# Performance work log

Measured on AMD Instinct MI355X. Metric: run time of the kernel, lower is better.

## Reference

```python
import math
import jax, jax.numpy as jnp
import numpy as np

HIDDEN = 256
FREQ = 256          # frequency_embedding_size
MASK_RATIO = 0.75
B, L, PD = 16, 4096, 512  # batch, num_patches, patch_dim = 2*16*16


def setup_inputs() -> dict:
    key = jax.random.key(0)
    ks = jax.random.split(key, 12)
    patches = jax.random.normal(ks[0], (B, L, PD), jnp.float32)
    # sorted segment ids -> contiguous segments per row (bincount/cumsum structure)
    sample_ids = jnp.sort(jax.random.randint(ks[1], (B, L), 0, 8), axis=1).astype(jnp.int32)
    effective_lens = (jax.random.randint(ks[2], (B,), 0, 2048) + L // 2).astype(jnp.int32)
    noise = jax.random.uniform(ks[3], (B, L), dtype=jnp.float32)
    fs = jax.random.uniform(ks[4], (B,), dtype=jnp.float32) * 1000.0
    W = jax.random.normal(ks[5], (HIDDEN, PD), jnp.float32) * 0.02   # projection.weight
    b = jnp.zeros((HIDDEN,), jnp.float32)                            # projection.bias
    pos = jax.random.normal(ks[6], (L, HIDDEN), jnp.float32) * 0.02  # position_embeddings
    w1 = jax.random.normal(ks[7], (HIDDEN, FREQ), jnp.float32) * 0.02
    b1 = jnp.zeros((HIDDEN,), jnp.float32)
    w2 = jax.random.normal(ks[8], (HIDDEN, HIDDEN), jnp.float32) * 0.02
    b2 = jnp.zeros((HIDDEN,), jnp.float32)
    return {"patches": patches, "sample_ids": sample_ids,
            "effective_lens": effective_lens, "noise": noise, "fs": fs,
            "W": W, "b": b, "pos": pos, "w1": w1, "b1": b1, "w2": w2, "b2": b2}


def timestep_embedding(t, dim=FREQ, max_period=10000.0):
    half = dim // 2
    freqs = jnp.exp(-math.log(max_period) * jnp.arange(half, dtype=jnp.float32) / half)
    args = t[:, None] * freqs[None, :]
    return jnp.concatenate([jnp.cos(args), jnp.sin(args)], axis=-1)  # [B, FREQ]


def reference(patches, sample_ids, effective_lens, noise, fs,
              W, b, pos, w1, b1, w2, b2):
    Bb, Ll, _ = patches.shape
    # patch projection + position embeddings
    emb = jnp.einsum('blp,hp->blh', patches, W) + b + pos[None]  # [B, L, H]
    # timestep (fs) embedding: Linear -> SiLU -> Linear
    t_freq = timestep_embedding(fs)
    fs_emb = jax.nn.silu(t_freq @ w1.T + b1) @ w2.T + b2  # [B, H]

    j = jnp.arange(Ll)[None, :]
    valid = j < effective_lens[:, None]                       # key-pad mask
    prev = jnp.concatenate([jnp.full((Bb, 1), -1, sample_ids.dtype),
                            sample_ids[:, :-1]], axis=1)
    seg_start = valid & (sample_ids != prev)                  # cls-token slots
    fs_tok = valid & jnp.concatenate([jnp.zeros((Bb, 1), bool),
                                      seg_start[:, :-1]], axis=1)  # fs-token slots
    # prefix (cls+fs) tokens get noise 0 -> always kept; padding -> inf
    nz = jnp.where(seg_start | fs_tok, 0.0, noise)
    nz = jnp.where(valid, nz, jnp.inf)

    num_samples = seg_start.sum(axis=1).astype(jnp.int32)
    keep_f = (effective_lens - 2 * num_samples).astype(jnp.float32) * (1.0 - MASK_RATIO)
    len_keep = 2 * num_samples + jnp.trunc(keep_f).astype(jnp.int32)

    ids_shuffle = jnp.argsort(nz, axis=1)                     # [B, L]
    keep = j < len_keep[:, None]
    # partial re-sort: sort first len_keep kept indices per row
    prefix_sorted = jnp.sort(jnp.where(keep, ids_shuffle, Ll), axis=1)
    ids_shuffle = jnp.where(keep, prefix_sorted, ids_shuffle)
    ids_restore = jnp.argsort(ids_shuffle, axis=1)

    gathered = jnp.take_along_axis(emb, ids_shuffle[..., None], axis=1)
    # fs conditioning added to kept tokens; padded (to L, masked) beyond len_keep
    seq_unmasked = jnp.where(keep[..., None], gathered + fs_emb[:, None, :], 0.0)

    mae_base = ((j >= len_keep[:, None]) & valid).astype(jnp.float32)
    mae_mask = jnp.take_along_axis(mae_base, ids_restore, axis=1)
    # fa2 path: no dense attn mask, just segment ids of kept tokens
    unmask_ids = jnp.where(keep,
                           jnp.take_along_axis(sample_ids, ids_shuffle, axis=1), -1)
    return seq_unmasked, mae_mask, ids_restore, unmask_ids
```

## Files before the change

### kernel.cpp

```cpp
#include <hip/hip_runtime.h>
#include <hip/hip_bf16.h>

#define BB 16
#define LL 4096
#define PDIM 512
#define HH 256
#define HALFD 128
#define MT 32

typedef short bf16x8 __attribute__((ext_vector_type(8)));
typedef float f32x4 __attribute__((ext_vector_type(4)));

__device__ __forceinline__ unsigned short f2bf(float f) {
  unsigned x = __float_as_uint(f);
  unsigned r = (x + 0x7FFFu + ((x >> 16) & 1u)) >> 16;
  return (unsigned short)r;
}

__device__ __forceinline__ unsigned long long make_key(
    const int* __restrict__ sid, const float* __restrict__ nrow, int eff, int j) {
  int s = sid[j];
  int sp = (j >= 1) ? sid[j - 1] : -1;
  int spp = (j >= 2) ? sid[j - 2] : -1;
  bool valid = j < eff;
  bool segs = valid && (s != sp);
  bool fst = valid && (j > 0) && (sp != spp);
  unsigned vb;
  if (!valid) vb = 0x7F800000u;
  else if (segs || fst) vb = 0u;
  else vb = __float_as_uint(nrow[j]);
  return (((unsigned long long)vb) << 32) | (unsigned)j;
}

__global__ __launch_bounds__(256) void prep_kernel(
    const float* __restrict__ W, unsigned short* __restrict__ Wbf,
    const float* __restrict__ fs, const float* __restrict__ w1,
    const float* __restrict__ b1, const float* __restrict__ w2,
    const float* __restrict__ b2, float* __restrict__ fs_emb) {
  __shared__ float tf[HH];
  __shared__ float hid[HH];
  if (blockIdx.x < 512) {
    int idx = blockIdx.x * 256 + threadIdx.x;
    Wbf[idx] = f2bf(W[idx]);
    return;
  }
  const int b = blockIdx.x - 512, h = threadIdx.x;
  float fv = fs[b];
  int i = h & (HALFD - 1);
  float freq = expf(-9.210340371976184f * (float)i / 128.0f);
  float arg = fv * freq;
  tf[h] = (h < HALFD) ? cosf(arg) : sinf(arg);
  __syncthreads();
  float acc = b1[h];
  const float* wr = w1 + (size_t)h * HH;
  for (int k = 0; k < HH; k += 4) {
    float4 w4 = *reinterpret_cast<const float4*>(&wr[k]);
    acc += tf[k] * w4.x + tf[k + 1] * w4.y + tf[k + 2] * w4.z + tf[k + 3] * w4.w;
  }
  hid[h] = acc / (1.0f + expf(-acc));
  __syncthreads();
  float acc2 = b2[h];
  const float* wr2 = w2 + (size_t)h * HH;
  for (int k = 0; k < HH; k += 4) {
    float4 w4 = *reinterpret_cast<const float4*>(&wr2[k]);
    acc2 += hid[k] * w4.x + hid[k + 1] * w4.y + hid[k + 2] * w4.z + hid[k + 3] * w4.w;
  }
  fs_emb[b * HH + h] = acc2;
}

__global__ __launch_bounds__(512) void rank_kernel(
    const int* __restrict__ sample_ids, const int* __restrict__ eff_lens,
    const float* __restrict__ noise, int* __restrict__ rank_part) {
  const int oq = blockIdx.x, os = blockIdx.y, b = blockIdx.z, tid = threadIdx.x;
  __shared__ __align__(16) unsigned long long sk[1024];
  const int eff = eff_lens[b];
  const int* sid = sample_ids + (size_t)b * LL;
  const float* nrow = noise + (size_t)b * LL;

  sk[tid] = make_key(sid, nrow, eff, os * 1024 + tid);
  sk[tid + 512] = make_key(sid, nrow, eff, os * 1024 + tid + 512);
  const int e0 = oq * 1024 + tid * 2;
  const unsigned long long k0 = make_key(sid, nrow, eff, e0);
  const unsigned long long k1 = make_key(sid, nrow, eff, e0 + 1);
  __syncthreads();

  int c0 = 0, c1 = 0;
#pragma unroll 8
  for (int k = 0; k < 1024; k += 2) {
    ulonglong2 kk = *reinterpret_cast<const ulonglong2*>(&sk[k]);
    c0 += (kk.x < k0) ? 1 : 0;
    c0 += (kk.y < k0) ? 1 : 0;
    c1 += (kk.x < k1) ? 1 : 0;
    c1 += (kk.y < k1) ? 1 : 0;
  }
  int2 res = make_int2(c0, c1);
  *reinterpret_cast<int2*>(&rank_part[((size_t)os * BB + b) * LL + e0]) = res;
}

__global__ __launch_bounds__(1024) void finalize_kernel(
    const int* __restrict__ sample_ids, const int* __restrict__ eff_lens,
    const int* __restrict__ rank_part, float* __restrict__ out_mae,
    float* __restrict__ out_restore, float* __restrict__ out_unmask,
    int* __restrict__ keep_idx, int* __restrict__ lk_arr) {
  const int b = blockIdx.x, tid = threadIdx.x;
  const int wid = tid >> 6, lane = tid & 63;
  __shared__ int wsum[16];
  __shared__ int lksh;
  const int eff = eff_lens[b];
  const int* sid = sample_ids + (size_t)b * LL;

  int local_ns = 0;
  for (int j = tid; j < LL; j += 1024) {
    int s = sid[j];
    int sp = (j >= 1) ? sid[j - 1] : -1;
    if (j < eff && s != sp) local_ns++;
  }
#pragma unroll
  for (int off = 32; off > 0; off >>= 1) local_ns += __shfl_down(local_ns, off);
  if (lane == 0) wsum[wid] = local_ns;
  __syncthreads();
  if (wid == 0) {
    int v = (lane < 16) ? wsum[lane] : 0;
#pragma unroll
    for (int off = 32; off > 0; off >>= 1) v += __shfl_down(v, off);
    if (lane == 0) {
      int ns = v;
      lksh = 2 * ns + ((eff - 2 * ns) >> 2);
    }
  }
  __syncthreads();
  const int lk = lksh;

  const int base = tid * 4;
  int4 p0 = *reinterpret_cast<const int4*>(&rank_part[((size_t)0 * BB + b) * LL + base]);
  int4 p1 = *reinterpret_cast<const int4*>(&rank_part[((size_t)1 * BB + b) * LL + base]);
  int4 p2 = *reinterpret_cast<const int4*>(&rank_part[((size_t)2 * BB + b) * LL + base]);
  int4 p3 = *reinterpret_cast<const int4*>(&rank_part[((size_t)3 * BB + b) * LL + base]);
  int r4[4] = {p0.x + p1.x + p2.x + p3.x, p0.y + p1.y + p2.y + p3.y,
               p0.z + p1.z + p2.z + p3.z, p0.w + p1.w + p2.w + p3.w};
  int c4[4], cnt = 0;
#pragma unroll
  for (int q = 0; q < 4; ++q) { c4[q] = (r4[q] < lk) ? 1 : 0; cnt += c4[q]; }

  int incl = cnt;
#pragma unroll
  for (int off = 1; off < 64; off <<= 1) {
    int v = __shfl_up(incl, off);
    if (lane >= off) incl += v;
  }
  if (lane == 63) wsum[wid] = incl;
  __syncthreads();
  if (wid == 0) {
    int s = (lane < 16) ? wsum[lane] : 0;
#pragma unroll
    for (int off = 1; off < 16; off <<= 1) {
      int v = __shfl_up(s, off);
      if (lane >= off) s += v;
    }
    if (lane < 16) wsum[lane] = s;
  }
  __syncthreads();
  int run = ((wid > 0) ? wsum[wid - 1] : 0) + incl - cnt;

  float4 rst, mmk;
  float* rp = &rst.x; float* mp = &mmk.x;
#pragma unroll
  for (int q = 0; q < 4; ++q) {
    int j = base + q;
    int r;
    if (c4[q]) {
      r = run;
      keep_idx[b * LL + run] = j;
      out_unmask[(size_t)b * LL + run] = (float)sid[j];
      run++;
    } else {
      r = r4[q];
    }
    rp[q] = (float)r;
    mp[q] = (r >= lk && r < eff) ? 1.0f : 0.0f;
  }
  *reinterpret_cast<float4*>(out_restore + (size_t)b * LL + base) = rst;
  *reinterpret_cast<float4*>(out_mae + (size_t)b * LL + base) = mmk;

  for (int p = tid; p < LL; p += 1024)
    if (p >= lk) out_unmask[(size_t)b * LL + p] = -1.0f;
  if (tid == 0) lk_arr[b] = lk;
}

__global__ __launch_bounds__(256) void proj_kernel(
    const float* __restrict__ patches, const unsigned short* __restrict__ Wbf,
    const float* __restrict__ bias, const float* __restrict__ pos,
    const float* __restrict__ fs_emb, const int* __restrict__ keep_idx,
    const int* __restrict__ lk_arr, float* __restrict__ out0) {
  const int tile = blockIdx.x, b = blockIdx.y, tid = threadIdx.x;
  const int p0 = tile * MT;
  int lk = lk_arr[b];
  lk = lk < 0 ? 0 : (lk > LL ? LL : lk);
  float* outB = out0 + ((size_t)b * LL + p0) * HH;
  int nt = lk - p0;
  nt = nt > MT ? MT : nt;

  if (nt <= 0) {
    float4 z = make_float4(0.f, 0.f, 0.f, 0.f);
    float4* o4 = reinterpret_cast<float4*>(outB);
#pragma unroll
    for (int i = 0; i < MT * HH / 4 / 256; ++i)
      o4[i * 256 + tid] = z;
    return;
  }

  __shared__ __align__(16) unsigned short pA[MT * 520];
  __shared__ int idxs[MT];
  if (tid < MT) idxs[tid] = (tid < nt) ? (keep_idx[b * LL + p0 + tid] & (LL - 1)) : 0;
  __syncthreads();

  {
    const int r = tid >> 3, kc = (tid & 7) * 64;
    const float* prow = patches + ((size_t)b * LL + (size_t)idxs[r]) * PDIM + kc;
#pragma unroll
    for (int i = 0; i < 16; ++i) {
      float4 v = reinterpret_cast<const float4*>(prow)[i];
      ushort4 u = make_ushort4(f2bf(v.x), f2bf(v.y), f2bf(v.z), f2bf(v.w));
      *reinterpret_cast<ushort4*>(&pA[r * 520 + kc + i * 4]) = u;
    }
  }
  __syncthreads();

  const int lane = tid & 63, w = tid >> 6;
  const int li = lane & 15, q = lane >> 4;
  f32x4 zero4 = {0.f, 0.f, 0.f, 0.f};
  f32x4 acc[2][4];
#pragma unroll
  for (int m = 0; m < 2; ++m)
#pragma unroll
    for (int n = 0; n < 4; ++n) acc[m][n] = zero4;

#pragma unroll 2
  for (int k0 = 0; k0 < PDIM; k0 += 32) {
    bf16x8 a0 = *reinterpret_cast<const bf16x8*>(&pA[li * 520 + k0 + q * 8]);
    bf16x8 a1 = *reinterpret_cast<const bf16x8*>(&pA[(16 + li) * 520 + k0 + q * 8]);
#pragma unroll
    for (int n = 0; n < 4; ++n) {
      bf16x8 bf = *reinterpret_cast<const bf16x8*>(
          &Wbf[(size_t)(w * 64 + n * 16 + li) * PDIM + k0 + q * 8]);
      acc[0][n] = __builtin_amdgcn_mfma_f32_16x16x32_bf16(a0, bf, acc[0][n], 0, 0, 0);
      acc[1][n] = __builtin_amdgcn_mfma_f32_16x16x32_bf16(a1, bf, acc[1][n], 0, 0, 0);
    }
  }

#pragma unroll
  for (int m = 0; m < 2; ++m) {
#pragma unroll
    for (int n = 0; n < 4; ++n) {
      const int col = w * 64 + n * 16 + li;
      const float bv = bias[col] + fs_emb[b * HH + col];
#pragma unroll
      for (int rr = 0; rr < 4; ++rr) {
        const int trow = m * 16 + q * 4 + rr;
        float val = 0.f;
        if (p0 + trow < lk)
          val = acc[m][n][rr] + bv + pos[(size_t)idxs[trow] * HH + col];
        outB[(size_t)trow * HH + col] = val;
      }
    }
  }
}

extern "C" void kernel_launch(void* const* d_in, const int* in_sizes, int n_in,
                              void* d_out, int out_size, void* d_ws, size_t ws_size,
                              hipStream_t stream) {
  const float* patches = (const float*)d_in[0];
  const int* sample_ids = (const int*)d_in[1];
  const int* eff = (const int*)d_in[2];
  const float* noise = (const float*)d_in[3];
  const float* fs = (const float*)d_in[4];
  const float* W = (const float*)d_in[5];
  const float* bias = (const float*)d_in[6];
  const float* pos = (const float*)d_in[7];
  const float* w1 = (const float*)d_in[8];
  const float* b1 = (const float*)d_in[9];
  const float* w2 = (const float*)d_in[10];
  const float* b2 = (const float*)d_in[11];

  float* out0 = (float*)d_out;
  float* out_mae = out0 + (size_t)BB * LL * HH;
  float* out_restore = out_mae + (size_t)BB * LL;
  float* out_unmask = out_restore + (size_t)BB * LL;

  char* ws = (char*)d_ws;
  unsigned short* Wbf = (unsigned short*)ws;
  float* fs_emb = (float*)(ws + 262144);
  int* keep_idx = (int*)(ws + 278528);
  int* rank_part = (int*)(ws + 540672);
  int* lk_arr = (int*)(ws + 1589248);
  if (ws_size < 1589312) return;

  prep_kernel<<<528, 256, 0, stream>>>(W, Wbf, fs, w1, b1, w2, b2, fs_emb);
  rank_kernel<<<dim3(4, 4, BB), 512, 0, stream>>>(sample_ids, eff, noise, rank_part);
  finalize_kernel<<<BB, 1024, 0, stream>>>(sample_ids, eff, rank_part, out_mae,
                                           out_restore, out_unmask, keep_idx, lk_arr);
  proj_kernel<<<dim3(LL / MT, BB), 256, 0, stream>>>(patches, Wbf, bias, pos,
                                                     fs_emb, keep_idx, lk_arr, out0);
}
```

Measured before the change: 310.8 us.

## Replace all-pairs rank with bucketed counting sort fused with prep kernel

Replaces the O(L^2) pairwise-comparison rank computation, which was split across many blocks with a partial-rank workspace, with a per-row bucket sort. Each row gets a shared-memory histogram over the noise value, a prefix scan, a scatter into buckets, and a local comparison inside each bucket. The weight conversion and timestep MLP are folded into the same launch, which removes two kernel launches and the rank_part global round trip. In exchange, rank work now depends on bucket occupancy: the zero-key bucket and any skewed noise bucket become serial inner loops in one block per row.

```diff
diff --git a/kernel.cpp b/kernel.cpp
--- a/kernel.cpp
+++ b/kernel.cpp
@@ -7,6 +7,7 @@
 #define HH 256
 #define HALFD 128
 #define MT 32
+#define NBUCK 257
 
 typedef short bf16x8 __attribute__((ext_vector_type(8)));
 typedef float f32x4 __attribute__((ext_vector_type(4)));
@@ -17,104 +18,141 @@
   return (unsigned short)r;
 }
 
-__device__ __forceinline__ unsigned long long make_key(
-    const int* __restrict__ sid, const float* __restrict__ nrow, int eff, int j) {
-  int s = sid[j];
-  int sp = (j >= 1) ? sid[j - 1] : -1;
-  int spp = (j >= 2) ? sid[j - 2] : -1;
-  bool valid = j < eff;
-  bool segs = valid && (s != sp);
-  bool fst = valid && (j > 0) && (sp != spp);
-  unsigned vb;
-  if (!valid) vb = 0x7F800000u;
-  else if (segs || fst) vb = 0u;
-  else vb = __float_as_uint(nrow[j]);
-  return (((unsigned long long)vb) << 32) | (unsigned)j;
-}
-
-__global__ __launch_bounds__(256) void prep_kernel(
+__global__ __launch_bounds__(1024) void sort_prep_kernel(
+    const int* __restrict__ sample_ids, const int* __restrict__ eff_lens,
+    const float* __restrict__ noise, float* __restrict__ out_mae,
+    float* __restrict__ out_restore, float* __restrict__ out_unmask,
+    int* __restrict__ keep_idx, int* __restrict__ lk_arr,
     const float* __restrict__ W, unsigned short* __restrict__ Wbf,
     const float* __restrict__ fs, const float* __restrict__ w1,
     const float* __restrict__ b1, const float* __restrict__ w2,
     const float* __restrict__ b2, float* __restrict__ fs_emb) {
+  __shared__ __align__(16) unsigned long long store[LL];
+  __shared__ int hist[NBUCK], cnt[NBUCK], bstart[NBUCK], bcur[NBUCK];
+  __shared__ int wsum[16];
+  __shared__ int lksh;
   __shared__ float tf[HH];
-  __shared__ float hid[HH];
-  if (blockIdx.x < 512) {
-    int idx = blockIdx.x * 256 + threadIdx.x;
-    Wbf[idx] = f2bf(W[idx]);
+  __shared__ float hidv[HH];
+
+  const int tid = threadIdx.x;
+
+  if (blockIdx.x >= 16) {
+    const int blk = blockIdx.x - 16;
+    if (blk < 128) {
+      const int idx = blk * 1024 + tid;
+      Wbf[idx] = f2bf(W[idx]);
+      return;
+    }
+    const int b = blk - 128, h = tid;
+    const float fv = fs[b];
+    if (h < HH) {
+      int i = h & (HALFD - 1);
+      float freq = expf(-9.210340371976184f * (float)i / 128.0f);
+      float arg = fv * freq;
+      tf[h] = (h < HALFD) ? cosf(arg) : sinf(arg);
+    }
+    __syncthreads();
+    if (h < HH) {
+      float acc = b1[h];
+      const float* wr = w1 + (size_t)h * HH;
+      for (int k = 0; k < HH; k += 4) {
+        float4 w4 = *reinterpret_cast<const float4*>(&wr[k]);
+        acc += tf[k] * w4.x + tf[k + 1] * w4.y + tf[k + 2] * w4.z + tf[k + 3] * w4.w;
+      }
+      hidv[h] = acc / (1.0f + expf(-acc));
+    }
+    __syncthreads();
+    if (h < HH) {
+      float acc2 = b2[h];
+      const float* wr2 = w2 + (size_t)h * HH;
+      for (int k = 0; k < HH; k += 4) {
+        float4 w4 = *reinterpret_cast<const float4*>(&wr2[k]);
+        acc2 += hidv[k] * w4.x + hidv[k + 1] * w4.y + hidv[k + 2] * w4.z + hidv[k + 3] * w4.w;
+      }
+      fs_emb[b * HH + h] = acc2;
+    }
     return;
   }
-  const int b = blockIdx.x - 512, h = threadIdx.x;
-  float fv = fs[b];
-  int i = h & (HALFD - 1);
-  float freq = expf(-9.210340371976184f * (float)i / 128.0f);
-  float arg = fv * freq;
-  tf[h] = (h < HALFD) ? cosf(arg) : sinf(arg);
-  __syncthreads();
-  float acc = b1[h];
-  const float* wr = w1 + (size_t)h * HH;
-  for (int k = 0; k < HH; k += 4) {
-    float4 w4 = *reinterpret_cast<const float4*>(&wr[k]);
-    acc += tf[k] * w4.x + tf[k + 1] * w4.y + tf[k + 2] * w4.z + tf[k + 3] * w4.w;
-  }
-  hid[h] = acc / (1.0f + expf(-acc));
-  __syncthreads();
-  float acc2 = b2[h];
-  const float* wr2 = w2 + (size_t)h * HH;
-  for (int k = 0; k < HH; k += 4) {
-    float4 w4 = *reinterpret_cast<const float4*>(&wr2[k]);
-    acc2 += hid[k] * w4.x + hid[k + 1] * w4.y + hid[k + 2] * w4.z + hid[k + 3] * w4.w;
-  }
-  fs_emb[b * HH + h] = acc2;
-}
-
-__global__ __launch_bounds__(512) void rank_kernel(
-    const int* __restrict__ sample_ids, const int* __restrict__ eff_lens,
-    const float* __restrict__ noise, int* __restrict__ rank_part) {
-  const int oq = blockIdx.x, os = blockIdx.y, b = blockIdx.z, tid = threadIdx.x;
-  __shared__ __align__(16) unsigned long long sk[1024];
+
+  const int b = blockIdx.x;
+  const int wid = tid >> 6, lane = tid & 63;
   const int eff = eff_lens[b];
   const int* sid = sample_ids + (size_t)b * LL;
-  const float* nrow = noise + (size_t)b * LL;
-
-  sk[tid] = make_key(sid, nrow, eff, os * 1024 + tid);
-  sk[tid + 512] = make_key(sid, nrow, eff, os * 1024 + tid + 512);
-  const int e0 = oq * 1024 + tid * 2;
-  const unsigned long long k0 = make_key(sid, nrow, eff, e0);
-  const unsigned long long k1 = make_key(sid, nrow, eff, e0 + 1);
-  __syncthreads();
-
-  int c0 = 0, c1 = 0;
-#pragma unroll 8
-  for (int k = 0; k < 1024; k += 2) {
-    ulonglong2 kk = *reinterpret_cast<const ulonglong2*>(&sk[k]);
-    c0 += (kk.x < k0) ? 1 : 0;
-    c0 += (kk.y < k0) ? 1 : 0;
-    c1 += (kk.x < k1) ? 1 : 0;
-    c1 += (kk.y < k1) ? 1 : 0;
-  }
-  int2 res = make_int2(c0, c1);
-  *reinterpret_cast<int2*>(&rank_part[((size_t)os * BB + b) * LL + e0]) = res;
-}
-
-__global__ __launch_bounds__(1024) void finalize_kernel(
-    const int* __restrict__ sample_ids, const int* __restrict__ eff_lens,
-    const int* __restrict__ rank_part, float* __restrict__ out_mae,
-    float* __restrict__ out_restore, float* __restrict__ out_unmask,
-    int* __restrict__ keep_idx, int* __restrict__ lk_arr) {
-  const int b = blockIdx.x, tid = threadIdx.x;
-  const int wid = tid >> 6, lane = tid & 63;
-  __shared__ int wsum[16];
-  __shared__ int lksh;
-  const int eff = eff_lens[b];
-  const int* sid = sample_ids + (size_t)b * LL;
-
-  int local_ns = 0;
-  for (int j = tid; j < LL; j += 1024) {
-    int s = sid[j];
-    int sp = (j >= 1) ? sid[j - 1] : -1;
-    if (j < eff && s != sp) local_ns++;
-  }
+  const int base = tid * 4;
+
+  int4 sv = *reinterpret_cast<const int4*>(&sid[base]);
+  float4 nv = *reinterpret_cast<const float4*>(&noise[(size_t)b * LL + base]);
+  const int sm1 = (base >= 1) ? sid[base - 1] : -1;
+  const int sm2 = (base >= 2) ? sid[base - 2] : -1;
+  const int svA[4] = {sv.x, sv.y, sv.z, sv.w};
+  const float nvA[4] = {nv.x, nv.y, nv.z, nv.w};
+
+  unsigned vbq[4];
+  int pbq[4];
+  bool invq[4];
+  int segsum = 0;
+#pragma unroll
+  for (int q = 0; q < 4; ++q) {
+    const int j = base + q;
+    const int s = svA[q];
+    const int sp = (q >= 1) ? svA[q - 1] : sm1;
+    const int spp = (q >= 2) ? svA[q - 2] : ((q == 1) ? sm1 : sm2);
+    const bool valid = j < eff;
+    const bool segs = valid && (s != sp);
+    const bool fst = valid && (j > 0) && (sp != spp);
+    segsum += segs ? 1 : 0;
+    invq[q] = !valid;
+    unsigned vb = (segs || fst) ? 0u : __float_as_uint(nvA[q]);
+    vbq[q] = vb;
+    pbq[q] = (vb == 0u) ? 0 : (1 + (int)(__uint_as_float(vb) * 256.0f));
+  }
+
+  if (tid < NBUCK) hist[tid] = 0;
+  __syncthreads();
+#pragma unroll
+  for (int q = 0; q < 4; ++q)
+    if (!invq[q]) atomicAdd(&hist[pbq[q]], 1);
+  __syncthreads();
+  if (tid < NBUCK) cnt[tid] = hist[tid];
+  __syncthreads();
+  for (int off = 1; off < NBUCK; off <<= 1) {
+    int v = 0;
+    if (tid < NBUCK && tid >= off) v = hist[tid - off];
+    __syncthreads();
+    if (tid < NBUCK) hist[tid] += v;
+    __syncthreads();
+  }
+  if (tid < NBUCK) {
+    const int st = hist[tid] - cnt[tid];
+    bstart[tid] = st;
+    bcur[tid] = st;
+  }
+  __syncthreads();
+#pragma unroll
+  for (int q = 0; q < 4; ++q)
+    if (!invq[q]) {
+      const int slot = atomicAdd(&bcur[pbq[q]], 1);
+      store[slot] = (((unsigned long long)vbq[q]) << 32) | (unsigned)(base + q);
+    }
+  __syncthreads();
+
+  int r4[4];
+#pragma unroll
+  for (int q = 0; q < 4; ++q) {
+    const int j = base + q;
+    if (invq[q]) {
+      r4[q] = j;
+      continue;
+    }
+    const int pb = pbq[q];
+    const int s0 = bstart[pb], c = cnt[pb];
+    const unsigned long long mykey = (((unsigned long long)vbq[q]) << 32) | (unsigned)j;
+    int cless = 0;
+    for (int t = 0; t < c; ++t) cless += (store[s0 + t] < mykey) ? 1 : 0;
+    r4[q] = s0 + cless;
+  }
+
+  int local_ns = segsum;
 #pragma unroll
   for (int off = 32; off > 0; off >>= 1) local_ns += __shfl_down(local_ns, off);
   if (lane == 0) wsum[wid] = local_ns;
@@ -124,25 +162,20 @@
 #pragma unroll
     for (int off = 32; off > 0; off >>= 1) v += __shfl_down(v, off);
     if (lane == 0) {
-      int ns = v;
+      const int ns = v;
       lksh = 2 * ns + ((eff - 2 * ns) >> 2);
     }
   }
   __syncthreads();
   const int lk = lksh;
 
-  const int base = tid * 4;
-  int4 p0 = *reinterpret_cast<const int4*>(&rank_part[((size_t)0 * BB + b) * LL + base]);
-  int4 p1 = *reinterpret_cast<const int4*>(&rank_part[((size_t)1 * BB + b) * LL + base]);
-  int4 p2 = *reinterpret_cast<const int4*>(&rank_part[((size_t)2 * BB + b) * LL + base]);
-  int4 p3 = *reinterpret_cast<const int4*>(&rank_part[((size_t)3 * BB + b) * LL + base]);
-  int r4[4] = {p0.x + p1.x + p2.x + p3.x, p0.y + p1.y + p2.y + p3.y,
-               p0.z + p1.z + p2.z + p3.z, p0.w + p1.w + p2.w + p3.w};
-  int c4[4], cnt = 0;
-#pragma unroll
-  for (int q = 0; q < 4; ++q) { c4[q] = (r4[q] < lk) ? 1 : 0; cnt += c4[q]; }
-
-  int incl = cnt;
+  int c4[4], cntk = 0;
+#pragma unroll
+  for (int q = 0; q < 4; ++q) {
+    c4[q] = (r4[q] < lk) ? 1 : 0;
+    cntk += c4[q];
+  }
+  int incl = cntk;
 #pragma unroll
   for (int off = 1; off < 64; off <<= 1) {
     int v = __shfl_up(incl, off);
@@ -160,18 +193,19 @@
     if (lane < 16) wsum[lane] = s;
   }
   __syncthreads();
-  int run = ((wid > 0) ? wsum[wid - 1] : 0) + incl - cnt;
+  int run = ((wid > 0) ? wsum[wid - 1] : 0) + incl - cntk;
 
   float4 rst, mmk;
-  float* rp = &rst.x; float* mp = &mmk.x;
+  float* rp = &rst.x;
+  float* mp = &mmk.x;
 #pragma unroll
   for (int q = 0; q < 4; ++q) {
-    int j = base + q;
+    const int j = base + q;
     int r;
     if (c4[q]) {
       r = run;
       keep_idx[b * LL + run] = j;
-      out_unmask[(size_t)b * LL + run] = (float)sid[j];
+      out_unmask[(size_t)b * LL + run] = (float)svA[q];
       run++;
     } else {
       r = r4[q];
@@ -291,14 +325,13 @@
   unsigned short* Wbf = (unsigned short*)ws;
   float* fs_emb = (float*)(ws + 262144);
   int* keep_idx = (int*)(ws + 278528);
-  int* rank_part = (int*)(ws + 540672);
-  int* lk_arr = (int*)(ws + 1589248);
-  if (ws_size < 1589312) return;
-
-  prep_kernel<<<528, 256, 0, stream>>>(W, Wbf, fs, w1, b1, w2, b2, fs_emb);
-  rank_kernel<<<dim3(4, 4, BB), 512, 0, stream>>>(sample_ids, eff, noise, rank_part);
-  finalize_kernel<<<BB, 1024, 0, stream>>>(sample_ids, eff, rank_part, out_mae,
-                                           out_restore, out_unmask, keep_idx, lk_arr);
+  int* lk_arr = (int*)(ws + 540672);
+  if (ws_size < 540736) return;
+
+  sort_prep_kernel<<<160, 1024, 0, stream>>>(sample_ids, eff, noise, out_mae,
+                                             out_restore, out_unmask, keep_idx,
+                                             lk_arr, W, Wbf, fs, w1, b1, w2, b2,
+                                             fs_emb);
   proj_kernel<<<dim3(LL / MT, BB), 256, 0, stream>>>(patches, Wbf, bias, pos,
                                                      fs_emb, keep_idx, lk_arr, out0);
 }
```

New measurement: 278.0 us. 1.12x faster.
